# Optimization experiments

Hardware: AMD Instinct MI355X
Metric: run time of the kernel (lower is better)

The kernel has to match this reference:

```python
import jax, jax.numpy as jnp
from jax import lax
import numpy as np

B, C_IN, H, W = 8, 1024, 64, 64
DI, C_OUT = 512, 1024
BN_EPS = 1e-5


def setup_inputs() -> dict:
    key = jax.random.key(0)
    ks = jax.random.split(key, 5)
    std = 0.01  # torch init.normal_(std=0.01)
    return {
        "x": jax.random.normal(ks[0], (B, C_IN, H, W), jnp.float32),
        "theta_w": jax.random.normal(ks[1], (DI, C_IN), jnp.float32) * std,
        "theta_b": jnp.zeros((DI,), jnp.float32),
        "phi_w": jax.random.normal(ks[2], (DI, C_IN), jnp.float32) * std,
        "phi_b": jnp.zeros((DI,), jnp.float32),
        "g_w": jax.random.normal(ks[3], (DI, C_IN), jnp.float32) * std,
        "g_b": jnp.zeros((DI,), jnp.float32),
        "out_w": jax.random.normal(ks[4], (C_OUT, DI), jnp.float32) * std,
        "out_b": jnp.zeros((C_OUT,), jnp.float32),
        "bn_w": jnp.ones((C_OUT,), jnp.float32),
        "bn_b": jnp.zeros((C_OUT,), jnp.float32),
    }


def _conv1x1(x, w, b):
    # x: [b,c,h,w], w: [o,c] -> [b,o,h,w]
    return jnp.einsum('bchw,oc->bohw', x, w) + b[None, :, None, None]


def reference(x, theta_w, theta_b, phi_w, phi_b, g_w, g_b, out_w, out_b, bn_w, bn_b):
    b, c, h, w = x.shape
    di = theta_w.shape[0]

    theta = _conv1x1(x, theta_w, theta_b).reshape(b, di, h * w)  # [b,di,N]

    # MaxPool2d(kernel=2, stride=2)
    pool = lax.reduce_window(x, -jnp.inf, lax.max,
                             (1, 1, 2, 2), (1, 1, 2, 2), 'VALID')
    phi = _conv1x1(pool, phi_w, phi_b).reshape(b, di, -1)   # [b,di,M]
    g = _conv1x1(pool, g_w, g_b).reshape(b, di, -1)          # [b,di,M]

    # scaled dot-product attention: scores [b,N,M]
    scores = jnp.einsum('bdn,bdm->bnm', theta, phi) * (di ** -0.5)
    p = jax.nn.softmax(scores, axis=-1)

    # t_x = g @ p^T  -> [b,di,N]
    t = jnp.einsum('bdm,bnm->bdn', g, p).reshape(b, di, h, w)

    y = _conv1x1(t, out_w, out_b)  # [b,C_out,h,w]

    # BatchNorm2d (training mode: batch statistics, biased variance)
    mean = jnp.mean(y, axis=(0, 2, 3), keepdims=True)
    var = jnp.var(y, axis=(0, 2, 3), keepdims=True)
    y = (y - mean) * lax.rsqrt(var + BN_EPS)
    y = y * bn_w[None, :, None, None] + bn_b[None, :, None, None]

    return y + x
```

## Files before the change

kernel.cpp:

```cpp
#include <hip/hip_runtime.h>
#include <cstdint>

typedef unsigned short u16;
typedef __attribute__((ext_vector_type(4))) unsigned short u16x4;
typedef __attribute__((ext_vector_type(8))) short short8;
typedef __attribute__((ext_vector_type(4))) float f32x4;

#define DI 512
#define CIN 1024
#define NPIX 4096
#define MPIX 1024

__device__ __forceinline__ float bf2f(u16 u) {
  union { unsigned int i; float f; } v; v.i = ((unsigned int)u) << 16; return v.f;
}
__device__ __forceinline__ u16 f2bf(float f) {
  union { float f; unsigned int i; } v; v.f = f;
  unsigned int r = v.i + 0x7fffu + ((v.i >> 16) & 1u);
  return (u16)(r >> 16);
}
__device__ __forceinline__ void unpack8(uint4 v, float* f) {
  union { unsigned int i; float f; } u;
  u.i = v.x << 16;          f[0] = u.f;
  u.i = v.x & 0xffff0000u;  f[1] = u.f;
  u.i = v.y << 16;          f[2] = u.f;
  u.i = v.y & 0xffff0000u;  f[3] = u.f;
  u.i = v.z << 16;          f[4] = u.f;
  u.i = v.z & 0xffff0000u;  f[5] = u.f;
  u.i = v.w << 16;          f[6] = u.f;
  u.i = v.w & 0xffff0000u;  f[7] = u.f;
}

__device__ __forceinline__ void gload16(const u16* g, u16* l) {
  __builtin_amdgcn_global_load_lds(
      (const __attribute__((address_space(1))) void*)g,
      (__attribute__((address_space(3))) void*)l, 16, 0, 0);
}

__global__ __launch_bounds__(256) void cvt4_kernel(
    const float* __restrict__ s0, const float* __restrict__ s1,
    const float* __restrict__ s2, const float* __restrict__ s3,
    u16* __restrict__ d0, u16* __restrict__ d1,
    u16* __restrict__ d2, u16* __restrict__ d3) {
  int i = blockIdx.x * 256 + threadIdx.x;
  int sel = i >> 17;
  int j = i & 131071;
  const float* src = sel == 0 ? s0 : sel == 1 ? s1 : sel == 2 ? s2 : s3;
  u16* dst = sel == 0 ? d0 : sel == 1 ? d1 : sel == 2 ? d2 : d3;
  float4 v = *(const float4*)(src + (long)j * 4);
  u16x4 w;
  w[0] = f2bf(v.x); w[1] = f2bf(v.y); w[2] = f2bf(v.z); w[3] = f2bf(v.w);
  *(u16x4*)(dst + (long)j * 4) = w;
}

__global__ __launch_bounds__(256) void transpose_pool_kernel(
    const float* __restrict__ x, u16* __restrict__ xT, u16* __restrict__ poolT) {
  __shared__ u16 tile[64][136];
  const int b = blockIdx.z;
  const int n0 = blockIdx.x * 128, c0 = blockIdx.y * 64;
  const float* xb = x + (long)b * CIN * NPIX;
  u16* xTb = xT + (long)b * NPIX * CIN;
  const int t = threadIdx.x;
  const int tc = t >> 5, tn = (t & 31) * 4;
  #pragma unroll
  for (int i = 0; i < 8; i++) {
    int c = tc + i * 8;
    float4 v = *(const float4*)(xb + (long)(c0 + c) * NPIX + n0 + tn);
    u16x4 w;
    w[0] = f2bf(v.x); w[1] = f2bf(v.y); w[2] = f2bf(v.z); w[3] = f2bf(v.w);
    *(u16x4*)&tile[c][tn] = w;
  }
  __syncthreads();
  const int tn2 = t >> 4, tc2 = (t & 15) * 4;
  #pragma unroll
  for (int i = 0; i < 8; i++) {
    int n = tn2 + i * 16;
    u16x4 w;
    w[0] = tile[tc2 + 0][n];
    w[1] = tile[tc2 + 1][n];
    w[2] = tile[tc2 + 2][n];
    w[3] = tile[tc2 + 3][n];
    *(u16x4*)(xTb + (long)(n0 + n) * CIN + c0 + tc2) = w;
  }
  const int j = t & 31, g = t >> 5;
  u16 r[8] __attribute__((aligned(16)));
  #pragma unroll
  for (int k = 0; k < 8; k++) {
    const int c = g * 8 + k;
    const unsigned d0 = *(const unsigned*)&tile[c][2 * j];
    const unsigned d1 = *(const unsigned*)&tile[c][64 + 2 * j];
    float m0 = fmaxf(bf2f((u16)(d0 & 0xffffu)), bf2f((u16)(d0 >> 16)));
    float m1 = fmaxf(bf2f((u16)(d1 & 0xffffu)), bf2f((u16)(d1 >> 16)));
    r[k] = f2bf(fmaxf(m0, m1));
  }
  *(uint4*)(poolT + ((long)b * MPIX + blockIdx.x * 32 + j) * CIN + c0 + g * 8) =
      *(uint4*)r;
}

template<int OM, bool HAS_BIAS, bool HAS_CS, bool HAS_SHIFT, bool HAS_EXP,
         bool HAS_PSUM2, bool HAS_CSP>
__global__ __launch_bounds__(256)
void gemm_tn(const u16* __restrict__ A, const u16* __restrict__ B,
             void* __restrict__ Cv, void* __restrict__ Cv2,
             const float* __restrict__ bias, const float* __restrict__ bias2,
             long sBias,
             const float* __restrict__ cs, long sCS,
             const float* __restrict__ shift, long sShift,
             float* __restrict__ psum_out,
             float scale, int M, int N, int K, long sA, long sB, long sC)
{
  A += blockIdx.z * sA;
  B += blockIdx.z * sB;
  if (HAS_BIAS) bias += blockIdx.z * sBias;
  if (HAS_CS || HAS_CSP) cs += blockIdx.z * sCS;
  if (HAS_SHIFT) shift += blockIdx.z * sShift;
  const int bm = blockIdx.y * 128;
  const int bn = blockIdx.x * 128;
  __shared__ __align__(16) u16 smem[128 * 128];
  u16* As = smem;
  u16* Bs = smem + 128 * 64;
  __shared__ float psum[4][128];
  const int tid = threadIdx.x;
  const int lane = tid & 63;
  const int wave = tid >> 6;
  const int wm = (wave >> 1) * 64;
  const int wn = (wave & 1) * 64;
  const int lr = lane & 15;
  const int q  = lane >> 4;
  const int sxor = lane & 7;
  const bool gps = (OM == 3) && (bm >= 512);
  f32x4 acc[4][4] = {};

  if (HAS_CSP) {
    if (tid < 128) {
      float s = 0.f;
      #pragma unroll
      for (int xx = 0; xx < 8; xx++) s += cs[xx * 4096 + bn + tid];
      psum[0][tid] = 1.0f / s;
    }
  }

  const int swz = ((lane & 7) ^ (lane >> 3)) * 8;
  const long grow = 32 * wave + (lane >> 3);
  const u16* Ag = A + ((long)bm + grow) * K + swz;
  const u16* Bg = B + ((long)bn + grow) * K + swz;

  for (int kt = 0; kt < K; kt += 64) {
    __syncthreads();
    #pragma unroll
    for (int i = 0; i < 4; i++) {
      gload16(Ag + (long)(8 * i) * K + kt, &As[(wave * 4 + i) * 512]);
      gload16(Bg + (long)(8 * i) * K + kt, &Bs[(wave * 4 + i) * 512]);
    }
    __syncthreads();
    #pragma unroll
    for (int kk = 0; kk < 2; kk++) {
      short8 av[4], bv[4];
      #pragma unroll
      for (int mi = 0; mi < 4; mi++)
        av[mi] = *(const short8*)&As[(wm + mi * 16 + lr) * 64 +
                                     (((kk << 2) + q) ^ sxor) * 8];
      #pragma unroll
      for (int ni = 0; ni < 4; ni++)
        bv[ni] = *(const short8*)&Bs[(wn + ni * 16 + lr) * 64 +
                                     (((kk << 2) + q) ^ sxor) * 8];
      #pragma unroll
      for (int mi = 0; mi < 4; mi++) {
        #pragma unroll
        for (int ni = 0; ni < 4; ni++)
          acc[mi][ni] = __builtin_amdgcn_mfma_f32_16x16x32_bf16(
              av[mi], bv[ni], acc[mi][ni], 0, 0, 0);
      }
    }
  }

  float invc[4];
  if (HAS_CSP) {
    #pragma unroll
    for (int ni = 0; ni < 4; ni++) invc[ni] = psum[0][wn + ni * 16 + lr];
  }
  __syncthreads();
  const int dr = (lane >> 4) * 4;
  const bool trans_out = (OM == 1) || (OM == 3 && !gps);
  float rowsum[4][4];
  float rowsq[4][4];
  if (HAS_EXP || HAS_PSUM2 || gps) {
    #pragma unroll
    for (int mi = 0; mi < 4; mi++)
      #pragma unroll
      for (int r = 0; r < 4; r++) { rowsum[mi][r] = 0.f; rowsq[mi][r] = 0.f; }
  }
  const float* bp = (OM == 3 && gps) ? bias2 - 512 : bias;
  #pragma unroll
  for (int mi = 0; mi < 4; mi++) {
    const int rowl = wm + mi * 16 + dr;
    const int rowb = bm + rowl;
    float bvs[4] = {0.f, 0.f, 0.f, 0.f};
    float shv[4] = {0.f, 0.f, 0.f, 0.f};
    if (HAS_BIAS) {
      #pragma unroll
      for (int r = 0; r < 4; r++) bvs[r] = bp[rowb + r];
    }
    if (HAS_SHIFT) {
      #pragma unroll
      for (int r = 0; r < 4; r++) shv[r] = shift[rowb + r];
    }
    #pragma unroll
    for (int ni = 0; ni < 4; ni++) {
      const int coll = wn + ni * 16 + lr;
      const float csv = HAS_CSP ? invc[ni] : (HAS_CS ? cs[bn + coll] : 1.0f);
      float v[4];
      #pragma unroll
      for (int r = 0; r < 4; r++) {
        float t = acc[mi][ni][r] * scale;
        if (HAS_CS || HAS_CSP) t *= csv;
        if (HAS_SHIFT) t -= shv[r];
        if (HAS_BIAS) t += bvs[r];
        if (HAS_EXP) t = expf(t);
        if (HAS_EXP || HAS_PSUM2 || gps) rowsum[mi][r] += t;
        if (HAS_PSUM2) rowsq[mi][r] += t * t;
        v[r] = t;
      }
      if (trans_out) {
        u16x4 w;
        #pragma unroll
        for (int r = 0; r < 4; r++) w[r] = f2bf(v[r]);
        unsigned bo = (unsigned)((coll * 128 + rowl) * 2) ^ ((coll & 7) << 4);
        *(u16x4*)((char*)smem + bo) = w;
      } else {
        #pragma unroll
        for (int r = 0; r < 4; r++) smem[(rowl + r) * 128 + coll] = f2bf(v[r]);
      }
    }
  }
  if (HAS_EXP || HAS_PSUM2 || gps) {
    #pragma unroll
    for (int msk = 1; msk < 16; msk <<= 1)
      #pragma unroll
      for (int mi = 0; mi < 4; mi++)
        #pragma unroll
        for (int r = 0; r < 4; r++) {
          rowsum[mi][r] += __shfl_xor(rowsum[mi][r], msk);
          if (HAS_PSUM2) rowsq[mi][r] += __shfl_xor(rowsq[mi][r], msk);
        }
    if ((lane & 15) == 0) {
      #pragma unroll
      for (int mi = 0; mi < 4; mi++)
        #pragma unroll
        for (int r = 0; r < 4; r++) {
          psum[wave & 1][wm + mi * 16 + dr + r] = rowsum[mi][r];
          if (HAS_PSUM2) psum[2 + (wave & 1)][wm + mi * 16 + dr + r] = rowsq[mi][r];
        }
    }
  }
  __syncthreads();
  if (trans_out) {
    const int Ms = (OM == 3) ? 512 : M;
    u16* C = (u16*)Cv + blockIdx.z * sC;
    #pragma unroll
    for (int i = 0; i < 8; i++) {
      const int chunk = i * 256 + tid;
      const int coll = chunk >> 4, rq = chunk & 15;
      unsigned bo = (unsigned)(coll * 256 + rq * 16) ^ ((coll & 7) << 4);
      uint4 w = *(const uint4*)((const char*)smem + bo);
      *(uint4*)(C + (long)(bn + coll) * Ms + bm + rq * 8) = w;
    }
  } else {
    u16* C = (OM == 3) ? (u16*)Cv2 + blockIdx.z * sC : (u16*)Cv + blockIdx.z * sC;
    const int rbase = (OM == 3) ? bm - 512 : bm;
    #pragma unroll
    for (int i = 0; i < 8; i++) {
      const int chunk = i * 256 + tid;
      const int row = chunk >> 4, cq = chunk & 15;
      uint4 w = *(const uint4*)(smem + row * 128 + cq * 8);
      *(uint4*)(C + (long)(rbase + row) * N + bn + cq * 8) = w;
    }
  }
  if (HAS_EXP || HAS_PSUM2 || gps) {
    if (tid < 128) {
      if (HAS_EXP)
        psum_out[((long)blockIdx.z * gridDim.x + blockIdx.x) * 4096 + bm + tid] =
            psum[0][tid] + psum[1][tid];
      if (HAS_PSUM2) {
        const long blk = ((long)blockIdx.z * gridDim.y + blockIdx.y) * gridDim.x
                         + blockIdx.x;
        psum_out[blk * 256 + tid] = psum[0][tid] + psum[1][tid];
        psum_out[blk * 256 + 128 + tid] = psum[2][tid] + psum[3][tid];
      }
      if (gps)
        psum_out[((long)blockIdx.z * gridDim.x + blockIdx.x) * 512 +
                 (bm - 512) + tid] = psum[0][tid] + psum[1][tid];
    }
  }
}

__global__ __launch_bounds__(256) void gbar_kernel(const float* __restrict__ g_ps,
                                                   float* __restrict__ gbar) {
  const int idx = blockIdx.x * 256 + threadIdx.x;
  const int b = idx >> 9, d = idx & 511;
  const float* p = g_ps + (long)b * 8 * 512 + d;
  float s = 0.f;
  #pragma unroll
  for (int xx = 0; xx < 8; xx++) s += p[(long)xx * 512];
  gbar[idx] = s * (1.0f / 1024.0f);
}

__global__ __launch_bounds__(256) void c0_kernel(const float* __restrict__ out_w,
                                                 const float* __restrict__ out_b,
                                                 const float* __restrict__ gbar,
                                                 float* __restrict__ c0) {
  const int idx = blockIdx.x * 4 + (threadIdx.x >> 6);
  const int lane = threadIdx.x & 63;
  const int b = idx >> 10, c = idx & 1023;
  const int d0 = lane * 8;
  float4 w0 = *(const float4*)(out_w + (long)c * DI + d0);
  float4 w1 = *(const float4*)(out_w + (long)c * DI + d0 + 4);
  float4 g0 = *(const float4*)(gbar + (long)b * DI + d0);
  float4 g1 = *(const float4*)(gbar + (long)b * DI + d0 + 4);
  float s = w0.x * g0.x + w0.y * g0.y + w0.z * g0.z + w0.w * g0.w
          + w1.x * g1.x + w1.y * g1.y + w1.z * g1.z + w1.w * g1.w;
  #pragma unroll
  for (int off = 32; off > 0; off >>= 1) s += __shfl_xor(s, off);
  if (lane == 0) c0[idx] = out_b[c] + s;
}

__global__ __launch_bounds__(256) void stats2_kernel(const float* __restrict__ partial,
                                                     const float* __restrict__ c0,
                                                     float* __restrict__ stats) {
  const int co = blockIdx.x * 256 + threadIdx.x;
  const int by = co >> 7, r = co & 127;
  float sd = 0.f, sd2 = 0.f, sbc = 0.f;
  for (int b = 0; b < 8; b++) {
    float sb = 0.f, qb = 0.f;
    #pragma unroll
    for (int bx = 0; bx < 32; bx++) {
      const long blk = (((long)b * 8 + by) * 32 + bx) * 256;
      sb += partial[blk + r];
      qb += partial[blk + 128 + r];
    }
    sd += sb; sd2 += qb;
    sbc += c0[b * 1024 + co] * sb;
  }
  float sc0 = 0.f, sc02 = 0.f;
  #pragma unroll
  for (int b = 0; b < 8; b++) {
    float c = c0[b * 1024 + co];
    sc0 += c; sc02 += c * c;
  }
  stats[co] = 4096.0f * sc0 + sd;
  stats[1024 + co] = 4096.0f * sc02 + 2.0f * sbc + sd2;
}

__global__ __launch_bounds__(256) void final_kernel(const u16* __restrict__ dy,
    const float* __restrict__ x, const float* __restrict__ stats,
    const float* __restrict__ c0,
    const float* __restrict__ bnw, const float* __restrict__ bnb,
    float* __restrict__ out) {
  const int bc = blockIdx.x;
  const int co = bc & 1023;
  const float mean = stats[co] * (1.0f / 32768.0f);
  const float var = stats[1024 + co] * (1.0f / 32768.0f) - mean * mean;
  const float inv = rsqrtf(var + 1e-5f) * bnw[co];
  const float addc = bnb[co] - mean * inv + c0[bc] * inv;
  const long base = (long)bc * 4096;
  const int t = threadIdx.x;
  #pragma unroll
  for (int i = 0; i < 2; i++) {
    const long off = base + (long)(i * 256 + t) * 8;
    uint4 v = *(const uint4*)(dy + off);
    float f[8]; unpack8(v, f);
    const float4 x0 = *(const float4*)(x + off);
    const float4 x1 = *(const float4*)(x + off + 4);
    float4 o0, o1;
    o0.x = f[0] * inv + addc + x0.x;
    o0.y = f[1] * inv + addc + x0.y;
    o0.z = f[2] * inv + addc + x0.z;
    o0.w = f[3] * inv + addc + x0.w;
    o1.x = f[4] * inv + addc + x1.x;
    o1.y = f[5] * inv + addc + x1.y;
    o1.z = f[6] * inv + addc + x1.z;
    o1.w = f[7] * inv + addc + x1.w;
    *(float4*)(out + off) = o0;
    *(float4*)(out + off + 4) = o1;
  }
}

extern "C" void kernel_launch(void* const* d_in, const int* in_sizes, int n_in,
                              void* d_out, int out_size, void* d_ws, size_t ws_size,
                              hipStream_t stream) {
  (void)in_sizes; (void)n_in; (void)out_size; (void)ws_size;
  const float* x       = (const float*)d_in[0];
  const float* theta_w = (const float*)d_in[1];
  const float* theta_b = (const float*)d_in[2];
  const float* phi_w   = (const float*)d_in[3];
  const float* phi_b   = (const float*)d_in[4];
  const float* g_w     = (const float*)d_in[5];
  const float* g_b     = (const float*)d_in[6];
  const float* out_w   = (const float*)d_in[7];
  const float* out_b   = (const float*)d_in[8];
  const float* bn_w    = (const float*)d_in[9];
  const float* bn_b    = (const float*)d_in[10];
  float* out = (float*)d_out;
  char* ws = (char*)d_ws;
  const size_t MB = 1024 * 1024;

  u16* xT     = (u16*)(ws + 0 * MB);
  u16* poolT  = (u16*)(ws + 64 * MB);
  u16* w_th   = (u16*)(ws + 80 * MB);
  u16* w_ph   = (u16*)(ws + 81 * MB);
  u16* w_g    = (u16*)(ws + 82 * MB);
  u16* thetaT = (u16*)(ws + 84 * MB);
  u16* phiT   = (u16*)(ws + 116 * MB);
  u16* g_n    = (u16*)(ws + 124 * MB);
  u16* e      = (u16*)(ws + 132 * MB);
  u16* tT     = (u16*)(ws + 196 * MB);
  u16* w_out  = (u16*)(ws + 228 * MB);
  float* gbar  = (float*)(ws + 229 * MB);
  float* c0b   = (float*)(ws + 229 * MB + 16384);
  float* stats = (float*)(ws + 229 * MB + 49152);
  float* partial = (float*)(ws + 230 * MB);
  float* partial2 = (float*)(ws + 231 * MB);
  float* g_ps = (float*)(ws + 233 * MB);
  u16* dy = xT;

  cvt4_kernel<<<2048, 256, 0, stream>>>(theta_w, phi_w, g_w, out_w,
                                        w_th, w_ph, w_g, w_out);
  transpose_pool_kernel<<<dim3(32, 16, 8), 256, 0, stream>>>(x, xT, poolT);
  gemm_tn<1, true, false, false, false, false, false>
      <<<dim3(32, 4, 8), 256, 0, stream>>>(
      w_th, xT, thetaT, nullptr, theta_b, nullptr, 0L, nullptr, 0L, nullptr, 0L,
      nullptr, 1.0f, 512, 4096, 1024, 0L, (long)NPIX * CIN, (long)NPIX * DI);
  gemm_tn<3, true, false, false, false, false, false>
      <<<dim3(8, 8, 8), 256, 0, stream>>>(
      w_ph, poolT, phiT, g_n, phi_b, g_b, 0L, nullptr, 0L, nullptr, 0L,
      g_ps, 1.0f, 1024, 1024, 1024, 0L, (long)MPIX * CIN, (long)MPIX * DI);
  gbar_kernel<<<16, 256, 0, stream>>>(g_ps, gbar);
  c0_kernel<<<2048, 256, 0, stream>>>(out_w, out_b, gbar, c0b);
  gemm_tn<0, false, false, false, true, false, false>
      <<<dim3(8, 32, 8), 256, 0, stream>>>(
      thetaT, phiT, e, nullptr, nullptr, nullptr, 0L, nullptr, 0L, nullptr, 0L,
      partial, 0.044194173824159216f, 4096, 1024, 512,
      (long)NPIX * DI, (long)MPIX * DI, (long)NPIX * MPIX);
  gemm_tn<1, false, false, true, false, false, true>
      <<<dim3(32, 4, 8), 256, 0, stream>>>(
      g_n, e, tT, nullptr, nullptr, nullptr, 0L, partial, 32768L, gbar, 512L,
      nullptr, 1.0f, 512, 4096, 1024,
      (long)DI * MPIX, (long)NPIX * MPIX, (long)NPIX * DI);
  gemm_tn<0, false, false, false, false, true, false>
      <<<dim3(32, 8, 8), 256, 0, stream>>>(
      w_out, tT, dy, nullptr, nullptr, nullptr, 0L, nullptr, 0L, nullptr, 0L,
      partial2, 1.0f, 1024, 4096, 512, 0L, (long)NPIX * DI, (long)1024 * NPIX);
  stats2_kernel<<<4, 256, 0, stream>>>(partial2, c0b, stats);
  final_kernel<<<8192, 256, 0, stream>>>(dy, x, stats, c0b, bn_w, bn_b, out);
}
```

Measured before the change: 356.0 us.

## Add 256x256-tile 512-thread GEMM kernel with double-buffered LDS for large GEMMs

Introduces a new gemm256 kernel that uses 256x256 output tiles, 8 waves per block and double-buffered shared memory with direct global-to-LDS loads and an XOR swizzle. The four large GEMMs (theta projection, scores with exp, g·p with softmax normalization, output projection with BN partial sums) switch to it. The stats reduction indexing is updated to match the new partial-sum layout. Larger tiles raise arithmetic intensity and cut global traffic per FLOP. The cost is fewer blocks (e.g. 256 blocks for some GEMMs), high register and LDS use, and possibly lower occupancy on 256 CUs.

```diff
diff --git a/kernel.cpp b/kernel.cpp
--- a/kernel.cpp
+++ b/kernel.cpp
@@ -95,6 +95,201 @@
   }
   *(uint4*)(poolT + ((long)b * MPIX + blockIdx.x * 32 + j) * CIN + c0 + g * 8) =
       *(uint4*)r;
+}
+
+template<int OM, bool HAS_BIAS, bool HAS_SHIFT, bool HAS_EXP, bool HAS_PSUM2,
+         bool HAS_CSP>
+__global__ __launch_bounds__(512, 2)
+void gemm256(const u16* __restrict__ A, const u16* __restrict__ B,
+             void* __restrict__ Cv,
+             const float* __restrict__ bias, long sBias,
+             const float* __restrict__ cs, long sCS,
+             const float* __restrict__ shift, long sShift,
+             float* __restrict__ psum_out,
+             float scale, int M, int N, int K, long sA, long sB, long sC)
+{
+  A += blockIdx.z * sA;
+  B += blockIdx.z * sB;
+  if (HAS_BIAS) bias += blockIdx.z * sBias;
+  if (HAS_CSP) cs += blockIdx.z * sCS;
+  if (HAS_SHIFT) shift += blockIdx.z * sShift;
+  const int bm = blockIdx.y * 256, bn = blockIdx.x * 256;
+  __shared__ __align__(16) u16 smem[65536];
+  __shared__ float psum[4][256];
+  __shared__ float psumq[4][256];
+  __shared__ float invs[256];
+  const int tid = threadIdx.x;
+  const int lane = tid & 63, wave = tid >> 6;
+  const int wr = wave >> 2, wc = wave & 3;
+  const int lr = lane & 15, q = lane >> 4, sx = lane & 7;
+  f32x4 acc[8][4] = {};
+
+  if (HAS_CSP && tid < 256) {
+    float ssum = 0.f;
+    #pragma unroll
+    for (int xx = 0; xx < 4; xx++) ssum += cs[xx * 4096 + bn + tid];
+    invs[tid] = 1.0f / ssum;
+  }
+
+  const int swz = ((lane & 7) ^ (lane >> 3)) * 8;
+  const long grow = 32 * wave + (lane >> 3);
+  const u16* Ag = A + ((long)bm + grow) * K + swz;
+  const u16* Bg = B + ((long)bn + grow) * K + swz;
+  const int niter = K >> 6;
+
+  #pragma unroll
+  for (int i = 0; i < 4; i++) {
+    gload16(Ag + (long)(8 * i) * K, &smem[(32 * wave + 8 * i) * 64]);
+    gload16(Bg + (long)(8 * i) * K, &smem[16384 + (32 * wave + 8 * i) * 64]);
+  }
+
+  for (int t = 0; t < niter; ++t) {
+    const int s = t & 1;
+    __builtin_amdgcn_s_barrier();
+    __builtin_amdgcn_sched_barrier(0);
+    if (t + 1 < niter) {
+      const long kofs = (long)(t + 1) * 64;
+      const int db = (s ^ 1) * 32768;
+      #pragma unroll
+      for (int i = 0; i < 4; i++) {
+        gload16(Ag + (long)(8 * i) * K + kofs, &smem[db + (32 * wave + 8 * i) * 64]);
+        gload16(Bg + (long)(8 * i) * K + kofs,
+                &smem[db + 16384 + (32 * wave + 8 * i) * 64]);
+      }
+      asm volatile("s_waitcnt vmcnt(8)" ::: "memory");
+    } else {
+      asm volatile("s_waitcnt vmcnt(0)" ::: "memory");
+    }
+    __builtin_amdgcn_s_barrier();
+    __builtin_amdgcn_sched_barrier(0);
+    const int bA = s * 32768, bB = s * 32768 + 16384;
+    #pragma unroll
+    for (int kk = 0; kk < 2; kk++) {
+      short8 bv[4];
+      #pragma unroll
+      for (int ci = 0; ci < 4; ci++)
+        bv[ci] = *(const short8*)&smem[bB + (wc * 64 + ci * 16 + lr) * 64 +
+                                       (((kk << 2) + q) ^ sx) * 8];
+      #pragma unroll
+      for (int ri = 0; ri < 8; ri++) {
+        short8 av = *(const short8*)&smem[bA + (wr * 128 + ri * 16 + lr) * 64 +
+                                          (((kk << 2) + q) ^ sx) * 8];
+        #pragma unroll
+        for (int ci = 0; ci < 4; ci++)
+          acc[ri][ci] = __builtin_amdgcn_mfma_f32_16x16x32_bf16(
+              av, bv[ci], acc[ri][ci], 0, 0, 0);
+      }
+    }
+  }
+  __syncthreads();
+
+  const int dr = (lane >> 4) * 4;
+  float invc[4];
+  if (HAS_CSP) {
+    #pragma unroll
+    for (int ci = 0; ci < 4; ci++) invc[ci] = invs[wc * 64 + ci * 16 + lr];
+  }
+  float rowsum[8][4], rowsq[8][4];
+  if (HAS_EXP || HAS_PSUM2) {
+    #pragma unroll
+    for (int ri = 0; ri < 8; ri++)
+      #pragma unroll
+      for (int r = 0; r < 4; r++) { rowsum[ri][r] = 0.f; rowsq[ri][r] = 0.f; }
+  }
+  #pragma unroll
+  for (int ri = 0; ri < 8; ri++) {
+    const int rowl = wr * 128 + ri * 16 + dr;
+    const int rowb = bm + rowl;
+    float bvs[4] = {0.f, 0.f, 0.f, 0.f};
+    float shv[4] = {0.f, 0.f, 0.f, 0.f};
+    if (HAS_BIAS) {
+      #pragma unroll
+      for (int r = 0; r < 4; r++) bvs[r] = bias[rowb + r];
+    }
+    if (HAS_SHIFT) {
+      #pragma unroll
+      for (int r = 0; r < 4; r++) shv[r] = shift[rowb + r];
+    }
+    #pragma unroll
+    for (int ci = 0; ci < 4; ci++) {
+      const int coll = wc * 64 + ci * 16 + lr;
+      float v[4];
+      #pragma unroll
+      for (int r = 0; r < 4; r++) {
+        float tv = acc[ri][ci][r] * scale;
+        if (HAS_CSP) tv *= invc[ci];
+        if (HAS_SHIFT) tv -= shv[r];
+        if (HAS_BIAS) tv += bvs[r];
+        if (HAS_EXP) tv = expf(tv);
+        if (HAS_EXP || HAS_PSUM2) rowsum[ri][r] += tv;
+        if (HAS_PSUM2) rowsq[ri][r] += tv * tv;
+        v[r] = tv;
+      }
+      if (OM == 1) {
+        u16x4 w;
+        #pragma unroll
+        for (int r = 0; r < 4; r++) w[r] = f2bf(v[r]);
+        unsigned bo = (unsigned)((coll * 256 + rowl) * 2) ^ ((coll & 7) << 4);
+        *(u16x4*)((char*)smem + bo) = w;
+      } else {
+        #pragma unroll
+        for (int r = 0; r < 4; r++) smem[(rowl + r) * 256 + coll] = f2bf(v[r]);
+      }
+    }
+  }
+  if (HAS_EXP || HAS_PSUM2) {
+    #pragma unroll
+    for (int msk = 1; msk < 16; msk <<= 1)
+      #pragma unroll
+      for (int ri = 0; ri < 8; ri++)
+        #pragma unroll
+        for (int r = 0; r < 4; r++) {
+          rowsum[ri][r] += __shfl_xor(rowsum[ri][r], msk);
+          if (HAS_PSUM2) rowsq[ri][r] += __shfl_xor(rowsq[ri][r], msk);
+        }
+    if ((lane & 15) == 0) {
+      #pragma unroll
+      for (int ri = 0; ri < 8; ri++)
+        #pragma unroll
+        for (int r = 0; r < 4; r++) {
+          psum[wc][wr * 128 + ri * 16 + dr + r] = rowsum[ri][r];
+          if (HAS_PSUM2) psumq[wc][wr * 128 + ri * 16 + dr + r] = rowsq[ri][r];
+        }
+    }
+  }
+  __syncthreads();
+  u16* C = (u16*)Cv + blockIdx.z * sC;
+  if (OM == 1) {
+    #pragma unroll
+    for (int i = 0; i < 16; i++) {
+      const int chunk = i * 512 + tid;
+      const int coll = chunk >> 5, rq = chunk & 31;
+      unsigned bo = (unsigned)(coll * 512 + rq * 16) ^ ((coll & 7) << 4);
+      uint4 w = *(const uint4*)((const char*)smem + bo);
+      *(uint4*)(C + (long)(bn + coll) * M + bm + rq * 8) = w;
+    }
+  } else {
+    #pragma unroll
+    for (int i = 0; i < 16; i++) {
+      const int chunk = i * 512 + tid;
+      const int row = chunk >> 5, cq = chunk & 31;
+      uint4 w = *(const uint4*)(smem + row * 256 + cq * 8);
+      *(uint4*)(C + (long)(bm + row) * N + bn + cq * 8) = w;
+    }
+  }
+  if ((HAS_EXP || HAS_PSUM2) && tid < 256) {
+    if (HAS_EXP)
+      psum_out[((long)blockIdx.z * gridDim.x + blockIdx.x) * 4096 + bm + tid] =
+          psum[0][tid] + psum[1][tid] + psum[2][tid] + psum[3][tid];
+    if (HAS_PSUM2) {
+      const long blk = ((long)blockIdx.z * gridDim.y + blockIdx.y) * gridDim.x
+                       + blockIdx.x;
+      psum_out[blk * 512 + tid] =
+          psum[0][tid] + psum[1][tid] + psum[2][tid] + psum[3][tid];
+      psum_out[blk * 512 + 256 + tid] =
+          psumq[0][tid] + psumq[1][tid] + psumq[2][tid] + psumq[3][tid];
+    }
+  }
 }
 
 template<int OM, bool HAS_BIAS, bool HAS_CS, bool HAS_SHIFT, bool HAS_EXP,
@@ -328,15 +523,15 @@
                                                      const float* __restrict__ c0,
                                                      float* __restrict__ stats) {
   const int co = blockIdx.x * 256 + threadIdx.x;
-  const int by = co >> 7, r = co & 127;
+  const int by = co >> 8, r = co & 255;
   float sd = 0.f, sd2 = 0.f, sbc = 0.f;
   for (int b = 0; b < 8; b++) {
     float sb = 0.f, qb = 0.f;
     #pragma unroll
-    for (int bx = 0; bx < 32; bx++) {
-      const long blk = (((long)b * 8 + by) * 32 + bx) * 256;
+    for (int bx = 0; bx < 16; bx++) {
+      const long blk = (((long)b * 4 + by) * 16 + bx) * 512;
       sb += partial[blk + r];
-      qb += partial[blk + 128 + r];
+      qb += partial[blk + 256 + r];
     }
     sd += sb; sd2 += qb;
     sbc += c0[b * 1024 + co] * sb;
@@ -426,30 +621,30 @@
   cvt4_kernel<<<2048, 256, 0, stream>>>(theta_w, phi_w, g_w, out_w,
                                         w_th, w_ph, w_g, w_out);
   transpose_pool_kernel<<<dim3(32, 16, 8), 256, 0, stream>>>(x, xT, poolT);
-  gemm_tn<1, true, false, false, false, false, false>
-      <<<dim3(32, 4, 8), 256, 0, stream>>>(
-      w_th, xT, thetaT, nullptr, theta_b, nullptr, 0L, nullptr, 0L, nullptr, 0L,
-      nullptr, 1.0f, 512, 4096, 1024, 0L, (long)NPIX * CIN, (long)NPIX * DI);
+  gemm256<1, true, false, false, false, false>
+      <<<dim3(16, 2, 8), 512, 0, stream>>>(
+      w_th, xT, thetaT, theta_b, 0L, nullptr, 0L, nullptr, 0L, nullptr,
+      1.0f, 512, 4096, 1024, 0L, (long)NPIX * CIN, (long)NPIX * DI);
   gemm_tn<3, true, false, false, false, false, false>
       <<<dim3(8, 8, 8), 256, 0, stream>>>(
       w_ph, poolT, phiT, g_n, phi_b, g_b, 0L, nullptr, 0L, nullptr, 0L,
       g_ps, 1.0f, 1024, 1024, 1024, 0L, (long)MPIX * CIN, (long)MPIX * DI);
   gbar_kernel<<<16, 256, 0, stream>>>(g_ps, gbar);
   c0_kernel<<<2048, 256, 0, stream>>>(out_w, out_b, gbar, c0b);
-  gemm_tn<0, false, false, false, true, false, false>
-      <<<dim3(8, 32, 8), 256, 0, stream>>>(
-      thetaT, phiT, e, nullptr, nullptr, nullptr, 0L, nullptr, 0L, nullptr, 0L,
-      partial, 0.044194173824159216f, 4096, 1024, 512,
+  gemm256<0, false, false, true, false, false>
+      <<<dim3(4, 16, 8), 512, 0, stream>>>(
+      thetaT, phiT, e, nullptr, 0L, nullptr, 0L, nullptr, 0L, partial,
+      0.044194173824159216f, 4096, 1024, 512,
       (long)NPIX * DI, (long)MPIX * DI, (long)NPIX * MPIX);
-  gemm_tn<1, false, false, true, false, false, true>
-      <<<dim3(32, 4, 8), 256, 0, stream>>>(
-      g_n, e, tT, nullptr, nullptr, nullptr, 0L, partial, 32768L, gbar, 512L,
-      nullptr, 1.0f, 512, 4096, 1024,
+  gemm256<1, false, true, false, false, true>
+      <<<dim3(16, 2, 8), 512, 0, stream>>>(
+      g_n, e, tT, nullptr, 0L, partial, 16384L, gbar, 512L, nullptr,
+      1.0f, 512, 4096, 1024,
       (long)DI * MPIX, (long)NPIX * MPIX, (long)NPIX * DI);
-  gemm_tn<0, false, false, false, false, true, false>
-      <<<dim3(32, 8, 8), 256, 0, stream>>>(
-      w_out, tT, dy, nullptr, nullptr, nullptr, 0L, nullptr, 0L, nullptr, 0L,
-      partial2, 1.0f, 1024, 4096, 512, 0L, (long)NPIX * DI, (long)1024 * NPIX);
+  gemm256<0, false, false, false, true, false>
+      <<<dim3(16, 4, 8), 512, 0, stream>>>(
+      w_out, tT, dy, nullptr, 0L, nullptr, 0L, nullptr, 0L, partial2,
+      1.0f, 1024, 4096, 512, 0L, (long)NPIX * DI, (long)1024 * NPIX);
   stats2_kernel<<<4, 256, 0, stream>>>(partial2, c0b, stats);
   final_kernel<<<8192, 256, 0, stream>>>(dy, x, stats, c0b, bn_w, bn_b, out);
 }
```

New measurement: 343.8 us. -3.4%, faster.
